# Performance work log

Hardware: AMD Instinct MI355X
Metric: run time of the kernel (lower is better)

Reference implementation:

```python
import jax, jax.numpy as jnp
import numpy as np

B, LQ, LK, D = 32, 1024, 1024, 256

def setup_inputs() -> dict:
    key = jax.random.key(0)
    ks = jax.random.split(key, 7)
    return {
        "raw_query": jax.random.normal(ks[0], (B, LQ, D), dtype=jnp.float32),
        "raw_key": jax.random.normal(ks[1], (B, LK, D), dtype=jnp.float32),
        "raw_value": jax.random.normal(ks[2], (B, LK, D), dtype=jnp.float32),
        "value_mask": jax.random.randint(ks[3], (B, LQ), 0, 2, dtype=jnp.int32),
        "WQ": jax.random.normal(ks[4], (D, D), dtype=jnp.float32) * 0.05,
        "WK": jax.random.normal(ks[5], (D, D), dtype=jnp.float32) * 0.05,
        "WV": jax.random.normal(ks[6], (D, D), dtype=jnp.float32) * 0.05,
    }

def reference(raw_query, raw_key, raw_value, value_mask, WQ, WK, WV):
    # Projections: [B, L, D] @ [D, D]
    Q = raw_query @ WQ
    K = raw_key @ WK
    V = raw_value @ WV
    # Scores: [B, LQ, LK] (use_scale=False -> no 1/sqrt(d_k))
    att = jnp.einsum("bqd,bkd->bqk", Q, K)
    # Mask expanded on axis=2 -> zeroes entire query rows of scores (faithful to tf.where+zeros_like)
    att = jnp.where(value_mask[:, :, None] > 0, att, jnp.zeros((), dtype=att.dtype))
    att = jax.nn.softmax(att, axis=-1)
    # Output: [B, LQ, D]
    return jnp.einsum("bqk,bkd->bqd", att, V)
```

## Files before the change

kernel.cpp:

```cpp
#include <hip/hip_runtime.h>
#include <hip/hip_bf16.h>
#include <math.h>

#define B_ 32
#define L_ 1024
#define D_ 256

typedef _Float16 half8 __attribute__((ext_vector_type(8)));
typedef __fp16   fp16x2 __attribute__((ext_vector_type(2)));
typedef short    s16x8 __attribute__((ext_vector_type(8)));
typedef float    f32x4 __attribute__((ext_vector_type(4)));

typedef __attribute__((address_space(3))) unsigned int lds_u32;
typedef __attribute__((address_space(1))) unsigned int gbl_u32;

__device__ __forceinline__ void gl_lds16(const void* g, void* l) {
    __builtin_amdgcn_global_load_lds((gbl_u32*)g, (lds_u32*)l, 16, 0, 0);
}

__device__ __forceinline__ unsigned short f2bf(float x) {
    unsigned u = __float_as_uint(x);
    u += 0x7FFFu + ((u >> 16) & 1u);
    return (unsigned short)(u >> 16);
}

__device__ __forceinline__ unsigned short f2h(float x) {
    _Float16 h = (_Float16)x;
    unsigned short u;
    __builtin_memcpy(&u, &h, 2);
    return u;
}

__device__ __forceinline__ unsigned pkrtz(float a, float b) {
    fp16x2 v = __builtin_amdgcn_cvt_pkrtz(a, b);
    unsigned u;
    __builtin_memcpy(&u, &v, 4);
    return u;
}

__global__ __launch_bounds__(256) void wprep_kernel(
    const float* __restrict__ W0, const float* __restrict__ W1,
    const float* __restrict__ W2, unsigned short* __restrict__ Wt)
{
    const int z = blockIdx.z;
    const float* __restrict__ W = (z == 0) ? W0 : (z == 1) ? W1 : W2;
    __shared__ unsigned short T[64][72];
    const int k0 = blockIdx.x << 6, n0 = blockIdx.y << 6;
    const int t = threadIdx.x;
    const int r = t >> 2, c0 = (t & 3) << 4;
    #pragma unroll
    for (int j = 0; j < 16; j += 4) {
        float4 w4 = *(const float4*)(W + (size_t)(k0 + r) * 256 + n0 + c0 + j);
        T[c0 + j + 0][r] = f2h(w4.x);
        T[c0 + j + 1][r] = f2h(w4.y);
        T[c0 + j + 2][r] = f2h(w4.z);
        T[c0 + j + 3][r] = f2h(w4.w);
    }
    __syncthreads();
    const int n = t >> 2, kc = (t & 3) << 4;
    unsigned short* dst = Wt + ((size_t)z << 16) + (size_t)(n0 + n) * 256 + k0 + kc;
    *(uint4*)(dst + 0) = *(const uint4*)&T[n][kc + 0];
    *(uint4*)(dst + 8) = *(const uint4*)&T[n][kc + 8];
}

__global__ __launch_bounds__(256) void proj_mfma_kernel(
    const float* __restrict__ A0, const float* __restrict__ A1,
    const float* __restrict__ A2, const unsigned short* __restrict__ Wt,
    unsigned short* __restrict__ Qh, unsigned short* __restrict__ Kh,
    unsigned short* __restrict__ Vt)
{
    __shared__ unsigned short SMEM[32768];
    unsigned short* Asm = SMEM;
    unsigned short* Bsm = SMEM + 16384;

    const int fblk = blockIdx.x;
    const int xcd = fblk & 7;
    const int g   = fblk >> 3;
    const int y   = g & 1;
    const int p   = g >> 1;
    const int z   = p >> 5;
    const int xl  = p & 31;
    const int xt  = (xcd << 5) + xl;
    const int bm = xt << 7, bn = y << 7;

    const float* __restrict__ A = (z == 0) ? A0 : (z == 1) ? A1 : A2;
    const int t = threadIdx.x, lane = t & 63, w = t >> 6;
    const int wm = (w >> 1) << 6, wn = (w & 1) << 6;

    const float* __restrict__ Ag = A + (size_t)bm * 256;
    const unsigned short* __restrict__ Bg = Wt + ((size_t)z << 16) + (size_t)bn * 256;

    f32x4 acc[4][4];
    const f32x4 z4 = {0.f, 0.f, 0.f, 0.f};
    #pragma unroll
    for (int mi = 0; mi < 4; ++mi)
        #pragma unroll
        for (int ni = 0; ni < 4; ++ni) acc[mi][ni] = z4;

    float4 aA[8], aB[8];

#define LOADA(itv, AR)                                                          \
    {                                                                           \
        _Pragma("unroll")                                                       \
        for (int i = 0; i < 8; ++i) {                                           \
            int r  = (t >> 4) + (i << 4);                                       \
            int c4 = t & 15;                                                    \
            AR[i] = *(const float4*)(Ag + (size_t)r * 256 + ((itv) << 6) + (c4 << 2)); \
        }                                                                       \
    }
#define WRITEA(buf, AR)                                                         \
    {                                                                           \
        _Pragma("unroll")                                                       \
        for (int i = 0; i < 8; ++i) {                                           \
            int r  = (t >> 4) + (i << 4);                                       \
            int c4 = t & 15;                                                    \
            unsigned h01 = pkrtz(AR[i].x, AR[i].y);                             \
            unsigned h23 = pkrtz(AR[i].z, AR[i].w);                             \
            int cs = (c4 >> 1) ^ (r & 7);                                       \
            uint2 d2; d2.x = h01; d2.y = h23;                                   \
            *(uint2*)&Asm[((buf) << 13) + (r << 6) + (cs << 3) + ((c4 & 1) << 2)] = d2; \
        }                                                                       \
    }

    auto stageB = [&](int buf, int it) {
        #pragma unroll
        for (int rr = 0; rr < 4; ++rr) {
            int o = (rr << 8) + t;
            int r = o >> 3, c = o & 7;
            int cs = c ^ (r & 7);
            gl_lds16(Bg + (size_t)r * 256 + (it << 6) + (cs << 3),
                     &Bsm[(buf << 13) + (o << 3)]);
        }
    };
    auto compute = [&](int buf) {
        #pragma unroll
        for (int kc = 0; kc < 2; ++kc) {
            half8 af[4], bfr[4];
            #pragma unroll
            for (int mi = 0; mi < 4; ++mi) {
                int m = wm + (mi << 4) + (lane & 15);
                int cs = ((kc << 2) + (lane >> 4)) ^ (m & 7);
                af[mi] = *(const half8*)&Asm[(buf << 13) + (m << 6) + (cs << 3)];
            }
            #pragma unroll
            for (int ni = 0; ni < 4; ++ni) {
                int n = wn + (ni << 4) + (lane & 15);
                int cs = ((kc << 2) + (lane >> 4)) ^ (n & 7);
                bfr[ni] = *(const half8*)&Bsm[(buf << 13) + (n << 6) + (cs << 3)];
            }
            #pragma unroll
            for (int mi = 0; mi < 4; ++mi)
                #pragma unroll
                for (int ni = 0; ni < 4; ++ni)
                    acc[mi][ni] = __builtin_amdgcn_mfma_f32_16x16x32_f16(
                        af[mi], bfr[ni], acc[mi][ni], 0, 0, 0);
        }
    };

    LOADA(0, aA);
    WRITEA(0, aA);
    stageB(0, 0);
    LOADA(1, aB);
    __syncthreads();

    LOADA(2, aA);
    WRITEA(1, aB);
    stageB(1, 1);
    compute(0);
    __syncthreads();
    LOADA(3, aB);
    WRITEA(0, aA);
    stageB(0, 2);
    compute(1);
    __syncthreads();
    WRITEA(1, aB);
    stageB(1, 3);
    compute(0);
    __syncthreads();
    compute(1);

#undef LOADA
#undef WRITEA

    if (z < 2) {
        unsigned short* __restrict__ C = (z == 0) ? Qh : Kh;
        #pragma unroll
        for (int mi = 0; mi < 4; ++mi) {
            int q = bm + wm + (mi << 4) + ((lane >> 4) << 2);
            #pragma unroll
            for (int ni = 0; ni < 4; ++ni) {
                int col = bn + wn + (ni << 4) + (lane & 15);
                #pragma unroll
                for (int r = 0; r < 4; ++r)
                    C[(size_t)(q + r) * 256 + col] = f2h(acc[mi][ni][r]);
            }
        }
    } else {
        __syncthreads();
        unsigned short (*Tt)[144] = (unsigned short(*)[144])SMEM;
        #pragma unroll
        for (int mi = 0; mi < 4; ++mi) {
            #pragma unroll
            for (int ni = 0; ni < 4; ++ni) {
                int n  = wn + (ni << 4) + (lane & 15);
                int m0 = wm + (mi << 4) + ((lane >> 4) << 2);
                ushort4 v;
                v.x = f2bf(acc[mi][ni][0]);
                v.y = f2bf(acc[mi][ni][1]);
                v.z = f2bf(acc[mi][ni][2]);
                v.w = f2bf(acc[mi][ni][3]);
                *(ushort4*)&Tt[n][m0] = v;
            }
        }
        __syncthreads();
        const int bb = bm >> 10, kin = bm & 1023;
        const int dr = t >> 1, cb = (t & 1) << 6;
        unsigned short* dst = Vt + ((size_t)bb * 256 + bn + dr) * 1024 + kin + cb;
        #pragma unroll
        for (int j = 0; j < 8; ++j)
            *(uint4*)(dst + (j << 3)) = *(const uint4*)&Tt[dr][cb + (j << 3)];
    }
}

__global__ __launch_bounds__(1024, 4) void fused_attn_kernel(
    const unsigned short* __restrict__ Qh, const unsigned short* __restrict__ Kh,
    const unsigned short* __restrict__ Vt, const int* __restrict__ mask,
    float* __restrict__ Out)
{
    __shared__ unsigned short Ks[2][16384];
    __shared__ unsigned short Vs[2][16384];
    __shared__ unsigned short Ps[128 * 64];
    float* lredp = (float*)Ps;

    const int f  = blockIdx.x;
    const int b  = (f & 7) + ((f >> 6) << 3);
    const int q0 = ((f >> 3) & 7) << 7;
    const size_t bL = (size_t)b * L_;
    const int t = threadIdx.x, lane = t & 63, w = t >> 6;
    const int wm_s = (w >> 1) << 4, wn_s = (w & 1) << 5;
    const int wm_v = (w >> 2) << 5, wn_v = (w & 3) << 6;

    const unsigned short* __restrict__ Kb = Kh + (bL << 8);
    const unsigned short* __restrict__ Vb = Vt + (bL << 8);

    auto stageK = [&](int buf, int kt) {
        #pragma unroll
        for (int i = 0; i < 2; ++i) {
            int o = (i << 10) + t;
            int r = o >> 5, c = o & 31;
            int cs = (c & 24) | ((c & 7) ^ (r & 7));
            gl_lds16(Kb + (size_t)((kt << 6) + r) * 256 + (cs << 3), &Ks[buf][o << 3]);
        }
    };
    auto stageV = [&](int buf, int kt) {
        #pragma unroll
        for (int i = 0; i < 2; ++i) {
            int o = (i << 10) + t;
            int d = o >> 3, c = o & 7;
            int cs = c ^ (d & 7);
            gl_lds16(Vb + ((size_t)d << 10) + (kt << 6) + (cs << 3), &Vs[buf][o << 3]);
        }
    };

    stageK(0, 0);
    stageV(0, 0);

    half8 qf[8];
    {
        int m = wm_s + (lane & 15);
        const unsigned short* qp = Qh + ((bL + q0 + m) << 8) + ((lane >> 4) << 3);
        #pragma unroll
        for (int kc = 0; kc < 8; ++kc)
            qf[kc] = *(const half8*)(qp + (kc << 5));
    }
    int mv[4];
    {
        int qrow = wm_s + ((lane >> 4) << 2);
        #pragma unroll
        for (int r = 0; r < 4; ++r) mv[r] = mask[bL + q0 + qrow + r];
    }

    f32x4 o_acc[2][4];
    const f32x4 z4 = {0.f, 0.f, 0.f, 0.f};
    #pragma unroll
    for (int mi = 0; mi < 2; ++mi)
        #pragma unroll
        for (int ni = 0; ni < 4; ++ni) o_acc[mi][ni] = z4;
    float lacc[4] = {};

    __syncthreads();

    for (int kt = 0; kt < 16; ++kt) {
        const int cur = kt & 1;
        if (kt < 15) stageV(cur ^ 1, kt + 1);

        f32x4 accs[2];
        accs[0] = z4; accs[1] = z4;
        #pragma unroll
        for (int kc = 0; kc < 8; ++kc) {
            int kb = (kc >> 1) << 6, cc = ((kc & 1) << 2) + (lane >> 4);
            int n0 = wn_s + (lane & 15);
            int n1 = n0 + 16;
            half8 bf0 = *(const half8*)&Ks[cur][(n0 << 8) + kb + ((cc ^ (n0 & 7)) << 3)];
            half8 bf1 = *(const half8*)&Ks[cur][(n1 << 8) + kb + ((cc ^ (n1 & 7)) << 3)];
            accs[0] = __builtin_amdgcn_mfma_f32_16x16x32_f16(qf[kc], bf0, accs[0], 0, 0, 0);
            accs[1] = __builtin_amdgcn_mfma_f32_16x16x32_f16(qf[kc], bf1, accs[1], 0, 0, 0);
        }

        {
            int qrow = wm_s + ((lane >> 4) << 2);
            #pragma unroll
            for (int ni = 0; ni < 2; ++ni) {
                int kl = wn_s + (ni << 4) + (lane & 15);
                #pragma unroll
                for (int r = 0; r < 4; ++r) {
                    int q = qrow + r;
                    float p = mv[r] ? __expf(accs[ni][r]) : 1.0f;
                    Ps[(q << 6) + ((((kl >> 3) ^ (q & 7)) << 3)) + (kl & 7)] = f2bf(p);
                    lacc[r] += p;
                }
            }
        }
        __syncthreads();

        if (kt < 15) stageK(cur ^ 1, kt + 1);

        #pragma unroll
        for (int kc2 = 0; kc2 < 2; ++kc2) {
            s16x8 pa[2], vb[4];
            int cc = (kc2 << 2) + (lane >> 4);
            #pragma unroll
            for (int mi = 0; mi < 2; ++mi) {
                int m = wm_v + (mi << 4) + (lane & 15);
                pa[mi] = *(const s16x8*)&Ps[(m << 6) + ((cc ^ (m & 7)) << 3)];
            }
            #pragma unroll
            for (int ni = 0; ni < 4; ++ni) {
                int n = wn_v + (ni << 4) + (lane & 15);
                vb[ni] = *(const s16x8*)&Vs[cur][(n << 6) + ((cc ^ (n & 7)) << 3)];
            }
            #pragma unroll
            for (int mi = 0; mi < 2; ++mi)
                #pragma unroll
                for (int ni = 0; ni < 4; ++ni)
                    o_acc[mi][ni] = __builtin_amdgcn_mfma_f32_16x16x32_bf16(
                        pa[mi], vb[ni], o_acc[mi][ni], 0, 0, 0);
        }
        __syncthreads();
    }

    #pragma unroll
    for (int r = 0; r < 4; ++r) {
        float v = lacc[r];
        v += __shfl_xor(v, 1);
        v += __shfl_xor(v, 2);
        v += __shfl_xor(v, 4);
        v += __shfl_xor(v, 8);
        if ((lane & 15) == 0)
            lredp[((wm_s + ((lane >> 4) << 2) + r) << 1) + (w & 1)] = v;
    }
    __syncthreads();

    #pragma unroll
    for (int mi = 0; mi < 2; ++mi) {
        #pragma unroll
        for (int rr = 0; rr < 4; ++rr) {
            int q = wm_v + (mi << 4) + ((lane >> 4) << 2) + rr;
            float inv = 1.0f / (lredp[q << 1] + lredp[(q << 1) + 1]);
            #pragma unroll
            for (int ni = 0; ni < 4; ++ni) {
                int d = wn_v + (ni << 4) + (lane & 15);
                Out[((bL + q0 + q) << 8) + d] = o_acc[mi][ni][rr] * inv;
            }
        }
    }
}

extern "C" void kernel_launch(void* const* d_in, const int* in_sizes, int n_in,
                              void* d_out, int out_size, void* d_ws, size_t ws_size,
                              hipStream_t stream) {
    const float* rq = (const float*)d_in[0];
    const float* rk = (const float*)d_in[1];
    const float* rv = (const float*)d_in[2];
    const int*   vm = (const int*)d_in[3];
    const float* WQ = (const float*)d_in[4];
    const float* WK = (const float*)d_in[5];
    const float* WV = (const float*)d_in[6];
    float* out = (float*)d_out;

    char* ws = (char*)d_ws;
    unsigned short* Qh = (unsigned short*)(ws);
    unsigned short* Kh = (unsigned short*)(ws + ((size_t)16 << 20));
    unsigned short* Vt = (unsigned short*)(ws + ((size_t)32 << 20));
    unsigned short* Wt = (unsigned short*)(ws + ((size_t)48 << 20));

    dim3 wg(4, 4, 3);
    wprep_kernel<<<wg, 256, 0, stream>>>(WQ, WK, WV, Wt);

    proj_mfma_kernel<<<1536, 256, 0, stream>>>(rq, rk, rv, Wt, Qh, Kh, Vt);

    fused_attn_kernel<<<256, 1024, 0, stream>>>(Qh, Kh, Vt, vm, out);
}
```

Measured before the change: 89.94 us.

## Load projection A fragments directly to registers and stage full weight tile once

The projection GEMM no longer stages activations through LDS. Each lane loads its own fp32 A fragment from global memory straight into registers and converts it to fp16 for MFMA. The whole 128x256 weight slice is loaded into LDS once up front with a swizzled layout, which removes the per-iteration syncthreads. The trade-off is uncoalesced row-strided global loads of A, with each wave reloading rows that other waves share, plus a deeper register double-buffer.

```diff
diff --git a/kernel.cpp b/kernel.cpp
--- a/kernel.cpp
+++ b/kernel.cpp
@@ -70,8 +70,7 @@
     unsigned short* __restrict__ Vt)
 {
     __shared__ unsigned short SMEM[32768];
-    unsigned short* Asm = SMEM;
-    unsigned short* Bsm = SMEM + 16384;
+    unsigned short* Wsm = SMEM;
 
     const int fblk = blockIdx.x;
     const int xcd = fblk & 7;
@@ -97,90 +96,67 @@
         #pragma unroll
         for (int ni = 0; ni < 4; ++ni) acc[mi][ni] = z4;
 
+    {
+        #pragma unroll
+        for (int i = 0; i < 16; ++i) {
+            int o = (i << 8) + t;
+            int r = o >> 5, c = o & 31;
+            int cs = (c & 24) | ((c & 7) ^ (r & 7));
+            gl_lds16(Bg + (size_t)r * 256 + (cs << 3), &Wsm[o << 3]);
+        }
+    }
+
     float4 aA[8], aB[8];
 
-#define LOADA(itv, AR)                                                          \
-    {                                                                           \
-        _Pragma("unroll")                                                       \
-        for (int i = 0; i < 8; ++i) {                                           \
-            int r  = (t >> 4) + (i << 4);                                       \
-            int c4 = t & 15;                                                    \
-            AR[i] = *(const float4*)(Ag + (size_t)r * 256 + ((itv) << 6) + (c4 << 2)); \
-        }                                                                       \
-    }
-#define WRITEA(buf, AR)                                                         \
-    {                                                                           \
-        _Pragma("unroll")                                                       \
-        for (int i = 0; i < 8; ++i) {                                           \
-            int r  = (t >> 4) + (i << 4);                                       \
-            int c4 = t & 15;                                                    \
-            unsigned h01 = pkrtz(AR[i].x, AR[i].y);                             \
-            unsigned h23 = pkrtz(AR[i].z, AR[i].w);                             \
-            int cs = (c4 >> 1) ^ (r & 7);                                       \
-            uint2 d2; d2.x = h01; d2.y = h23;                                   \
-            *(uint2*)&Asm[((buf) << 13) + (r << 6) + (cs << 3) + ((c4 & 1) << 2)] = d2; \
-        }                                                                       \
-    }
-
-    auto stageB = [&](int buf, int it) {
-        #pragma unroll
-        for (int rr = 0; rr < 4; ++rr) {
-            int o = (rr << 8) + t;
-            int r = o >> 3, c = o & 7;
-            int cs = c ^ (r & 7);
-            gl_lds16(Bg + (size_t)r * 256 + (it << 6) + (cs << 3),
-                     &Bsm[(buf << 13) + (o << 3)]);
+    auto loadA = [&](int kcv, float4 (&AR)[8]) {
+        #pragma unroll
+        for (int mi = 0; mi < 4; ++mi) {
+            const float* ap = Ag + (size_t)(wm + (mi << 4) + (lane & 15)) * 256
+                              + (kcv << 5) + ((lane >> 4) << 3);
+            AR[2 * mi]     = *(const float4*)ap;
+            AR[2 * mi + 1] = *(const float4*)(ap + 4);
         }
     };
-    auto compute = [&](int buf) {
-        #pragma unroll
-        for (int kc = 0; kc < 2; ++kc) {
-            half8 af[4], bfr[4];
-            #pragma unroll
-            for (int mi = 0; mi < 4; ++mi) {
-                int m = wm + (mi << 4) + (lane & 15);
-                int cs = ((kc << 2) + (lane >> 4)) ^ (m & 7);
-                af[mi] = *(const half8*)&Asm[(buf << 13) + (m << 6) + (cs << 3)];
-            }
-            #pragma unroll
-            for (int ni = 0; ni < 4; ++ni) {
-                int n = wn + (ni << 4) + (lane & 15);
-                int cs = ((kc << 2) + (lane >> 4)) ^ (n & 7);
-                bfr[ni] = *(const half8*)&Bsm[(buf << 13) + (n << 6) + (cs << 3)];
-            }
-            #pragma unroll
-            for (int mi = 0; mi < 4; ++mi)
-                #pragma unroll
-                for (int ni = 0; ni < 4; ++ni)
-                    acc[mi][ni] = __builtin_amdgcn_mfma_f32_16x16x32_f16(
-                        af[mi], bfr[ni], acc[mi][ni], 0, 0, 0);
-        }
+    auto kstep = [&](int kcv, float4 (&AR)[8], int nextkc) {
+        half8 af[4];
+        #pragma unroll
+        for (int mi = 0; mi < 4; ++mi) {
+            unsigned hh[4];
+            hh[0] = pkrtz(AR[2 * mi].x,     AR[2 * mi].y);
+            hh[1] = pkrtz(AR[2 * mi].z,     AR[2 * mi].w);
+            hh[2] = pkrtz(AR[2 * mi + 1].x, AR[2 * mi + 1].y);
+            hh[3] = pkrtz(AR[2 * mi + 1].z, AR[2 * mi + 1].w);
+            __builtin_memcpy(&af[mi], hh, 16);
+        }
+        if (nextkc >= 0) loadA(nextkc, AR);
+        half8 bfr[4];
+        int ch = (kcv << 2) + (lane >> 4);
+        #pragma unroll
+        for (int ni = 0; ni < 4; ++ni) {
+            int n = wn + (ni << 4) + (lane & 15);
+            int cs = (ch & 24) | ((ch & 7) ^ (n & 7));
+            bfr[ni] = *(const half8*)&Wsm[(n << 8) + (cs << 3)];
+        }
+        #pragma unroll
+        for (int mi = 0; mi < 4; ++mi)
+            #pragma unroll
+            for (int ni = 0; ni < 4; ++ni)
+                acc[mi][ni] = __builtin_amdgcn_mfma_f32_16x16x32_f16(
+                    af[mi], bfr[ni], acc[mi][ni], 0, 0, 0);
     };
 
-    LOADA(0, aA);
-    WRITEA(0, aA);
-    stageB(0, 0);
-    LOADA(1, aB);
+    loadA(0, aA);
+    loadA(1, aB);
     __syncthreads();
 
-    LOADA(2, aA);
-    WRITEA(1, aB);
-    stageB(1, 1);
-    compute(0);
-    __syncthreads();
-    LOADA(3, aB);
-    WRITEA(0, aA);
-    stageB(0, 2);
-    compute(1);
-    __syncthreads();
-    WRITEA(1, aB);
-    stageB(1, 3);
-    compute(0);
-    __syncthreads();
-    compute(1);
-
-#undef LOADA
-#undef WRITEA
+    kstep(0, aA, 2);
+    kstep(1, aB, 3);
+    kstep(2, aA, 4);
+    kstep(3, aB, 5);
+    kstep(4, aA, 6);
+    kstep(5, aB, 7);
+    kstep(6, aA, -1);
+    kstep(7, aB, -1);
 
     if (z < 2) {
         unsigned short* __restrict__ C = (z == 0) ? Qh : Kh;
```

Measured after the change: 110.8 us. +23.2%, slower.

## Double projection block threads, shrink per-wave tile, stage Q/K stores through LDS

Applied to the files above, without the earlier changes.

The projection GEMM now runs 512 threads (8 waves) per block. Each wave computes a 32x64 tile instead of 64x64, which halves the accumulator and prefetch registers to allow more resident waves. The A-load pattern is reorganised so each thread loads a contiguous 64-byte row segment and writes 16-byte LDS chunks. Q/K outputs are now staged through LDS and written with coalesced 16-byte stores instead of scattered 2-byte global writes. The trade-off is extra barriers and LDS traffic in the epilogue.

```diff
diff --git a/kernel.cpp b/kernel.cpp
--- a/kernel.cpp
+++ b/kernel.cpp
@@ -63,7 +63,7 @@
     *(uint4*)(dst + 8) = *(const uint4*)&T[n][kc + 8];
 }
 
-__global__ __launch_bounds__(256) void proj_mfma_kernel(
+__global__ __launch_bounds__(512, 4) void proj_mfma_kernel(
     const float* __restrict__ A0, const float* __restrict__ A1,
     const float* __restrict__ A2, const unsigned short* __restrict__ Wt,
     unsigned short* __restrict__ Qh, unsigned short* __restrict__ Kh,
@@ -85,47 +85,47 @@
 
     const float* __restrict__ A = (z == 0) ? A0 : (z == 1) ? A1 : A2;
     const int t = threadIdx.x, lane = t & 63, w = t >> 6;
-    const int wm = (w >> 1) << 6, wn = (w & 1) << 6;
+    const int wm = (w >> 1) << 5, wn = (w & 1) << 6;
 
     const float* __restrict__ Ag = A + (size_t)bm * 256;
     const unsigned short* __restrict__ Bg = Wt + ((size_t)z << 16) + (size_t)bn * 256;
 
-    f32x4 acc[4][4];
+    f32x4 acc[2][4];
     const f32x4 z4 = {0.f, 0.f, 0.f, 0.f};
     #pragma unroll
-    for (int mi = 0; mi < 4; ++mi)
+    for (int mi = 0; mi < 2; ++mi)
         #pragma unroll
         for (int ni = 0; ni < 4; ++ni) acc[mi][ni] = z4;
 
-    float4 aA[8], aB[8];
+    const int ar = t >> 2, ac4 = t & 3;
+    float4 aA[4], aB[4];
 
 #define LOADA(itv, AR)                                                          \
     {                                                                           \
         _Pragma("unroll")                                                       \
-        for (int i = 0; i < 8; ++i) {                                           \
-            int r  = (t >> 4) + (i << 4);                                       \
-            int c4 = t & 15;                                                    \
-            AR[i] = *(const float4*)(Ag + (size_t)r * 256 + ((itv) << 6) + (c4 << 2)); \
-        }                                                                       \
+        for (int i = 0; i < 4; ++i)                                             \
+            AR[i] = *(const float4*)(Ag + (size_t)ar * 256 + ((itv) << 6)       \
+                                     + (ac4 << 4) + (i << 2));                  \
     }
 #define WRITEA(buf, AR)                                                         \
     {                                                                           \
         _Pragma("unroll")                                                       \
-        for (int i = 0; i < 8; ++i) {                                           \
-            int r  = (t >> 4) + (i << 4);                                       \
-            int c4 = t & 15;                                                    \
-            unsigned h01 = pkrtz(AR[i].x, AR[i].y);                             \
-            unsigned h23 = pkrtz(AR[i].z, AR[i].w);                             \
-            int cs = (c4 >> 1) ^ (r & 7);                                       \
-            uint2 d2; d2.x = h01; d2.y = h23;                                   \
-            *(uint2*)&Asm[((buf) << 13) + (r << 6) + (cs << 3) + ((c4 & 1) << 2)] = d2; \
+        for (int i = 0; i < 2; ++i) {                                           \
+            int c  = (ac4 << 1) + i;                                            \
+            int cs = c ^ (ar & 7);                                              \
+            uint4 d;                                                            \
+            d.x = pkrtz(AR[2 * i].x,     AR[2 * i].y);                          \
+            d.y = pkrtz(AR[2 * i].z,     AR[2 * i].w);                          \
+            d.z = pkrtz(AR[2 * i + 1].x, AR[2 * i + 1].y);                      \
+            d.w = pkrtz(AR[2 * i + 1].z, AR[2 * i + 1].w);                      \
+            *(uint4*)&Asm[((buf) << 13) + (ar << 6) + (cs << 3)] = d;           \
         }                                                                       \
     }
 
     auto stageB = [&](int buf, int it) {
         #pragma unroll
-        for (int rr = 0; rr < 4; ++rr) {
-            int o = (rr << 8) + t;
+        for (int i = 0; i < 2; ++i) {
+            int o = (i << 9) + t;
             int r = o >> 3, c = o & 7;
             int cs = c ^ (r & 7);
             gl_lds16(Bg + (size_t)r * 256 + (it << 6) + (cs << 3),
@@ -135,9 +135,9 @@
     auto compute = [&](int buf) {
         #pragma unroll
         for (int kc = 0; kc < 2; ++kc) {
-            half8 af[4], bfr[4];
-            #pragma unroll
-            for (int mi = 0; mi < 4; ++mi) {
+            half8 af[2], bfr[4];
+            #pragma unroll
+            for (int mi = 0; mi < 2; ++mi) {
                 int m = wm + (mi << 4) + (lane & 15);
                 int cs = ((kc << 2) + (lane >> 4)) ^ (m & 7);
                 af[mi] = *(const half8*)&Asm[(buf << 13) + (m << 6) + (cs << 3)];
@@ -149,7 +149,7 @@
                 bfr[ni] = *(const half8*)&Bsm[(buf << 13) + (n << 6) + (cs << 3)];
             }
             #pragma unroll
-            for (int mi = 0; mi < 4; ++mi)
+            for (int mi = 0; mi < 2; ++mi)
                 #pragma unroll
                 for (int ni = 0; ni < 4; ++ni)
                     acc[mi][ni] = __builtin_amdgcn_mfma_f32_16x16x32_f16(
@@ -184,40 +184,47 @@
 
     if (z < 2) {
         unsigned short* __restrict__ C = (z == 0) ? Qh : Kh;
-        #pragma unroll
-        for (int mi = 0; mi < 4; ++mi) {
-            int q = bm + wm + (mi << 4) + ((lane >> 4) << 2);
+        __syncthreads();
+        unsigned short (*Cs)[136] = (unsigned short(*)[136])SMEM;
+        #pragma unroll
+        for (int mi = 0; mi < 2; ++mi) {
+            int q0l = wm + (mi << 4) + ((lane >> 4) << 2);
             #pragma unroll
             for (int ni = 0; ni < 4; ++ni) {
-                int col = bn + wn + (ni << 4) + (lane & 15);
+                int cl = wn + (ni << 4) + (lane & 15);
                 #pragma unroll
                 for (int r = 0; r < 4; ++r)
-                    C[(size_t)(q + r) * 256 + col] = f2h(acc[mi][ni][r]);
-            }
+                    Cs[q0l + r][cl] = f2h(acc[mi][ni][r]);
+            }
+        }
+        __syncthreads();
+        #pragma unroll
+        for (int i = 0; i < 4; ++i) {
+            int o = (i << 9) + t;
+            int r = o >> 4, c = o & 15;
+            *(uint4*)(C + (size_t)(bm + r) * 256 + bn + (c << 3)) =
+                *(const uint4*)&Cs[r][c << 3];
         }
     } else {
         __syncthreads();
         unsigned short (*Tt)[144] = (unsigned short(*)[144])SMEM;
         #pragma unroll
-        for (int mi = 0; mi < 4; ++mi) {
+        for (int mi = 0; mi < 2; ++mi) {
+            int m0 = wm + (mi << 4) + ((lane >> 4) << 2);
             #pragma unroll
             for (int ni = 0; ni < 4; ++ni) {
-                int n  = wn + (ni << 4) + (lane & 15);
-                int m0 = wm + (mi << 4) + ((lane >> 4) << 2);
-                ushort4 v;
-                v.x = f2bf(acc[mi][ni][0]);
-                v.y = f2bf(acc[mi][ni][1]);
-                v.z = f2bf(acc[mi][ni][2]);
-                v.w = f2bf(acc[mi][ni][3]);
-                *(ushort4*)&Tt[n][m0] = v;
+                int n = wn + (ni << 4) + (lane & 15);
+                #pragma unroll
+                for (int r = 0; r < 4; ++r)
+                    Tt[n][m0 + r] = f2bf(acc[mi][ni][r]);
             }
         }
         __syncthreads();
         const int bb = bm >> 10, kin = bm & 1023;
-        const int dr = t >> 1, cb = (t & 1) << 6;
+        const int dr = t >> 2, cb = (t & 3) << 5;
         unsigned short* dst = Vt + ((size_t)bb * 256 + bn + dr) * 1024 + kin + cb;
         #pragma unroll
-        for (int j = 0; j < 8; ++j)
+        for (int j = 0; j < 4; ++j)
             *(uint4*)(dst + (j << 3)) = *(const uint4*)&Tt[dr][cb + (j << 3)];
     }
 }
@@ -397,7 +404,7 @@
     dim3 wg(4, 4, 3);
     wprep_kernel<<<wg, 256, 0, stream>>>(WQ, WK, WV, Wt);
 
-    proj_mfma_kernel<<<1536, 256, 0, stream>>>(rq, rk, rv, Wt, Qh, Kh, Vt);
+    proj_mfma_kernel<<<1536, 512, 0, stream>>>(rq, rk, rv, Wt, Qh, Kh, Vt);
 
     fused_attn_kernel<<<256, 1024, 0, stream>>>(Qh, Kh, Vt, vm, out);
 }
```

After: 89.89 us, median of 2. Within noise of the previous version (-0.1%).
